# Kernel optimization log

Hardware: AMD Instinct MI355X
Metric: run time of the kernel (lower is better)

## Reference

```python
import jax, jax.numpy as jnp
import numpy as np

B, N, E, H = 4, 2048, 1024, 16
D = E // H
SCALE = D ** -0.5
EPS = 1.1920929e-07  # torch.finfo(float32).eps (RMSNorm default eps=None)


def _rmsnorm(x, w):
    # normalize over last dim (head_dim)
    ms = jnp.mean(x * x, axis=-1, keepdims=True)
    return x * jax.lax.rsqrt(ms + EPS) * w


def setup_inputs() -> dict:
    key = jax.random.key(0)
    ks = jax.random.split(key, 10)
    s_in = E ** -0.5
    return {
        "hidden_states": jax.random.normal(ks[0], (B, N, E), jnp.float32),
        "encoder_hidden_states": jax.random.normal(ks[1], (B, N, E), jnp.float32),
        "Wq": jax.random.normal(ks[2], (E, E), jnp.float32) * s_in,
        "bq": jnp.zeros((E,), jnp.float32),
        "Wkv": jax.random.normal(ks[3], (E, 2 * E), jnp.float32) * s_in,
        "bkv": jnp.zeros((2 * E,), jnp.float32),
        "qn_w": jnp.ones((D,), jnp.float32),
        "kn_w": jnp.ones((D,), jnp.float32),
        "Wo": jax.random.normal(ks[4], (E, E), jnp.float32) * s_in,
        "bo": jnp.zeros((E,), jnp.float32),
    }


def reference(hidden_states, encoder_hidden_states, Wq, bq, Wkv, bkv, qn_w, kn_w, Wo, bo):
    q_proj = hidden_states @ Wq + bq                     # [B,N,E]
    kv_proj = encoder_hidden_states @ Wkv + bkv          # [B,N,2E]
    qkv = jnp.concatenate([q_proj, kv_proj], axis=-1)    # [B,N,3E]
    # Rearrange 'b n (h d j) -> b h n d j' with j=3 innermost: interleaved split
    qkv = qkv.reshape(B, N, H, D, 3)
    q = jnp.transpose(qkv[..., 0], (0, 2, 1, 3)) * SCALE  # [B,H,N,D]
    k = jnp.transpose(qkv[..., 1], (0, 2, 1, 3))
    v = jnp.transpose(qkv[..., 2], (0, 2, 1, 3))
    q = _rmsnorm(q, qn_w)
    k = _rmsnorm(k, kn_w)
    # q already pre-scaled (before norm, which cancels it up to eps); attention uses no extra scale
    scores = jnp.einsum('bhqd,bhkd->bhqk', q, k)          # [B,H,N,N]
    attn = jax.nn.softmax(scores, axis=-1)
    ctx = jnp.einsum('bhqk,bhkd->bhqd', attn, v)          # [B,H,N,D]
    ctx = jnp.transpose(ctx, (0, 2, 1, 3)).reshape(B, N, E)
    return ctx @ Wo + bo
```

## Files before the change

### kernel.cpp

```cpp
#include <hip/hip_runtime.h>
#include <hip/hip_bf16.h>
#include <cstddef>
#include <cmath>

#define B_ 4
#define N_ 2048
#define E_ 1024
#define H_ 16
#define D_ 64
#define SCALE_ 0.125f
#define EPS_ 1.1920929e-07f

typedef __attribute__((ext_vector_type(8))) short short8;
typedef __attribute__((ext_vector_type(4))) short short4s;
typedef __attribute__((ext_vector_type(4))) float floatx4;

__device__ __forceinline__ unsigned short f2bf(float x) {
    unsigned int u = __float_as_uint(x);
    u += 0x7FFFu + ((u >> 16) & 1u);
    return (unsigned short)(u >> 16);
}
__device__ __forceinline__ float bf2f(unsigned short b) {
    return __uint_as_float(((unsigned int)b) << 16);
}

#define MFMA16(a, b, c) __builtin_amdgcn_mfma_f32_16x16x32_bf16((a), (b), (c), 0, 0, 0)

__global__ __launch_bounds__(256) void aprep_kernel(float* __restrict__ x)
{
    const size_t i = ((size_t)blockIdx.x * 256 + threadIdx.x) * 4;
    float4 v = *(const float4*)(x + i);
    float vx[4] = {v.x, v.y, v.z, v.w};
    short8 p;
#pragma unroll
    for (int c = 0; c < 4; ++c) {
        unsigned short hb = f2bf(vx[c]);
        p[2 * c]     = (short)hb;
        p[2 * c + 1] = (short)f2bf(vx[c] - bf2f(hb));
    }
    *(short8*)(x + i) = p;
}

__global__ __launch_bounds__(256) void wtrans_kernel(
    const float* __restrict__ src, int K, int N,
    short* __restrict__ dstH, short* __restrict__ dstL)
{
    __shared__ __align__(16) short Hs[64][68], Ls[64][68];
    const int k0 = blockIdx.x * 64, n0 = blockIdx.y * 64;
    const int t = threadIdx.x;
    {
        int kk = t >> 4, cc = (t & 15) * 4;
#pragma unroll
        for (int i = 0; i < 4; ++i) {
            int k = kk + i * 16;
            float4 v = *(const float4*)(src + (size_t)(k0 + k) * N + n0 + cc);
            float vx[4] = {v.x, v.y, v.z, v.w};
            short4s h4, l4;
#pragma unroll
            for (int c = 0; c < 4; ++c) {
                unsigned short hb = f2bf(vx[c]);
                h4[c] = (short)hb;
                l4[c] = (short)f2bf(vx[c] - bf2f(hb));
            }
            *(short4s*)&Hs[k][cc] = h4;
            *(short4s*)&Ls[k][cc] = l4;
        }
    }
    __syncthreads();
    {
        int nn = t >> 3, kq = (t & 7) * 8;
#pragma unroll
        for (int i = 0; i < 2; ++i) {
            int n = nn + i * 32;
            short8 h8, l8;
#pragma unroll
            for (int j = 0; j < 8; ++j) { h8[j] = Hs[kq + j][n]; l8[j] = Ls[kq + j][n]; }
            *(short8*)(dstH + (size_t)(n0 + n) * K + k0 + kq) = h8;
            *(short8*)(dstL + (size_t)(n0 + n) * K + k0 + kq) = l8;
        }
    }
}

__global__ __launch_bounds__(256) void proj_kernel(
    const short* __restrict__ hs_pk, const short* __restrict__ ehs_pk,
    const short* __restrict__ WtqH, const short* __restrict__ WtqL,
    const short* __restrict__ WtkvH, const short* __restrict__ WtkvL,
    const float* __restrict__ bq, const float* __restrict__ bkv,
    short* __restrict__ qh, short* __restrict__ ql,
    short* __restrict__ kh, short* __restrict__ kl,
    short* __restrict__ vt)
{
    const int ct = blockIdx.x;
    const int rt = blockIdx.y;
    const int col0 = ct * 128;
    const bool isQ = (col0 < 1024);
    const short* __restrict__ Apk  = (isQ ? hs_pk : ehs_pk) + (size_t)rt * 128 * 1024 * 2;
    const short* __restrict__ WH   = isQ ? WtqH : WtkvH;
    const short* __restrict__ WL   = isQ ? WtqL : WtkvL;
    const float* __restrict__ bias = isQ ? bq : bkv;
    const int wcol0 = isQ ? col0 : (col0 - 1024);

    __shared__ __align__(16) short Ah[128 * 40], Al[128 * 40];
    __shared__ __align__(16) short Bh[128 * 40], Bl[128 * 40];

    const int tid = threadIdx.x;
    const int lane = tid & 63, wid = tid >> 6;
    const int wr = wid >> 1, wc = wid & 1;
    const int l15 = lane & 15, g = lane >> 4;

    floatx4 acc[4][4];
#pragma unroll
    for (int m = 0; m < 4; ++m)
#pragma unroll
        for (int n = 0; n < 4; ++n) acc[m][n] = floatx4{0.f, 0.f, 0.f, 0.f};

    short8 rA[4], rBh[2], rBl[2];

    auto LOAD = [&](int k0) {
#pragma unroll
        for (int i = 0; i < 4; ++i) {
            int f = tid + i * 256;
            int row = f >> 3, kq = f & 7;
            rA[i] = *(const short8*)(Apk + ((size_t)row * 1024 + k0 + kq * 4) * 2);
        }
#pragma unroll
        for (int i = 0; i < 2; ++i) {
            int f = tid + i * 256;
            int colb = f >> 2, kq = (f & 3) * 8;
            rBh[i] = *(const short8*)(WH + (size_t)(wcol0 + colb) * 1024 + k0 + kq);
            rBl[i] = *(const short8*)(WL + (size_t)(wcol0 + colb) * 1024 + k0 + kq);
        }
    };
    auto STORE = [&]() {
#pragma unroll
        for (int i = 0; i < 4; ++i) {
            int f = tid + i * 256;
            int row = f >> 3, kq = f & 7;
            short4s h4, l4;
#pragma unroll
            for (int c = 0; c < 4; ++c) { h4[c] = rA[i][2 * c]; l4[c] = rA[i][2 * c + 1]; }
            *(short4s*)&Ah[row * 40 + kq * 4] = h4;
            *(short4s*)&Al[row * 40 + kq * 4] = l4;
        }
#pragma unroll
        for (int i = 0; i < 2; ++i) {
            int f = tid + i * 256;
            int colb = f >> 2, kq = (f & 3) * 8;
            *(short8*)&Bh[colb * 40 + kq] = rBh[i];
            *(short8*)&Bl[colb * 40 + kq] = rBl[i];
        }
    };
    auto COMPUTE = [&]() {
        short8 ah[4], al[4], bh[4], bl[4];
#pragma unroll
        for (int m = 0; m < 4; ++m) {
            int r = (wr * 64 + m * 16 + l15) * 40 + g * 8;
            ah[m] = *(const short8*)&Ah[r];
            al[m] = *(const short8*)&Al[r];
        }
#pragma unroll
        for (int n = 0; n < 4; ++n) {
            int r = (wc * 64 + n * 16 + l15) * 40 + g * 8;
            bh[n] = *(const short8*)&Bh[r];
            bl[n] = *(const short8*)&Bl[r];
        }
#pragma unroll
        for (int m = 0; m < 4; ++m)
#pragma unroll
            for (int n = 0; n < 4; ++n) {
                acc[m][n] = MFMA16(ah[m], bh[n], acc[m][n]);
                acc[m][n] = MFMA16(ah[m], bl[n], acc[m][n]);
                acc[m][n] = MFMA16(al[m], bh[n], acc[m][n]);
            }
    };

    LOAD(0);
    STORE();
    __syncthreads();
    for (int k0 = 32; k0 < 1024; k0 += 32) {
        LOAD(k0);
        COMPUTE();
        __syncthreads();
        STORE();
        __syncthreads();
    }
    COMPUTE();

#pragma unroll
    for (int n = 0; n < 4; ++n) {
        int c = col0 + wc * 64 + n * 16 + l15;
        float bi = bias[c - (isQ ? 0 : 1024)];
        int h   = c / 192;
        int rem = c - h * 192;
        int dd  = rem / 3;
        int j3  = rem - dd * 3;
#pragma unroll
        for (int m = 0; m < 4; ++m) {
            int grow0 = rt * 128 + wr * 64 + m * 16 + g * 4;
            int b = grow0 >> 11, nn0 = grow0 & 2047;
            if (j3 == 2) {
                short4s v4;
#pragma unroll
                for (int r = 0; r < 4; ++r) v4[r] = (short)f2bf(acc[m][n][r] + bi);
                *(short4s*)(vt + (((size_t)b * 16 + h) * 64 + dd) * 2048 + nn0) = v4;
            } else {
                short* dh = (j3 == 0) ? qh : kh;
                short* dl = (j3 == 0) ? ql : kl;
#pragma unroll
                for (int r = 0; r < 4; ++r) {
                    float val = acc[m][n][r] + bi;
                    size_t idx = (((size_t)b * 16 + h) * 2048 + (nn0 + r)) * 64 + dd;
                    unsigned short hb = f2bf(val);
                    dh[idx] = (short)hb;
                    dl[idx] = (short)f2bf(val - bf2f(hb));
                }
            }
        }
    }
}

__global__ __launch_bounds__(256) void rmsnorm_kernel(
    short* __restrict__ qh, short* __restrict__ ql,
    short* __restrict__ kh, short* __restrict__ kl,
    const float* __restrict__ qn_w, const float* __restrict__ kn_w)
{
    const int tid = threadIdx.x, lane = tid & 63, wid = tid >> 6;
    const size_t row = (size_t)blockIdx.x * 16 + wid * 4 + (lane >> 4);
    const int d4 = (lane & 15) * 4;
    const bool isQ = (blockIdx.y == 0);
    short* xh = (isQ ? qh : kh) + row * 64 + d4;
    short* xl = (isQ ? ql : kl) + row * 64 + d4;
    const float* w = (isQ ? qn_w : kn_w) + d4;

    short4s h4 = *(short4s*)xh, l4 = *(short4s*)xl;
    float x[4];
#pragma unroll
    for (int c = 0; c < 4; ++c) {
        x[c] = bf2f((unsigned short)h4[c]) + bf2f((unsigned short)l4[c]);
        if (isQ) x[c] *= SCALE_;
    }
    float s = x[0]*x[0] + x[1]*x[1] + x[2]*x[2] + x[3]*x[3];
#pragma unroll
    for (int off = 1; off <= 8; off <<= 1) s += __shfl_xor(s, off);
    float r = rsqrtf(s * (1.f / 64.f) + EPS_);
#pragma unroll
    for (int c = 0; c < 4; ++c) {
        float y = x[c] * r * w[c];
        unsigned short hb = f2bf(y);
        h4[c] = (short)hb;
        l4[c] = (short)f2bf(y - bf2f(hb));
    }
    *(short4s*)xh = h4;
    *(short4s*)xl = l4;
}

__global__ __launch_bounds__(256) void attn_kernel(
    const short* __restrict__ qh, const short* __restrict__ ql,
    const short* __restrict__ kh, const short* __restrict__ kl,
    const short* __restrict__ vt,
    short* __restrict__ cxh, short* __restrict__ cxl)
{
    const int bh = blockIdx.x;
    const int qt = blockIdx.y;
    const size_t kbase = (size_t)bh * 2048 * 64;
    const size_t vbase = (size_t)bh * 64 * 2048;

    __shared__ __align__(16) short Kh[64 * 72], Kl[64 * 72];
    __shared__ __align__(16) short Vs[64 * 72];
    __shared__ __align__(16) short Ps[64 * 72];

    const int tid = threadIdx.x;
    const int lane = tid & 63, wid = tid >> 6;
    const int l15 = lane & 15, g = lane >> 4;

    const size_t qrow0 = ((size_t)bh * 2048 + qt * 64 + wid * 16 + l15) * 64;
    short8 qfh[2], qfl[2];
#pragma unroll
    for (int s = 0; s < 2; ++s) {
        qfh[s] = *(const short8*)(qh + qrow0 + s * 32 + g * 8);
        qfl[s] = *(const short8*)(ql + qrow0 + s * 32 + g * 8);
    }

    short8 rKh[2], rKl[2], rV[2];
    auto LOADKV = [&](int kt) {
#pragma unroll
        for (int i = 0; i < 2; ++i) {
            int f = tid + i * 256;
            int row = f >> 3, dq = (f & 7) * 8;
            const size_t gsrc = kbase + (size_t)(kt * 64 + row) * 64 + dq;
            rKh[i] = *(const short8*)(kh + gsrc);
            rKl[i] = *(const short8*)(kl + gsrc);
        }
#pragma unroll
        for (int i = 0; i < 2; ++i) {
            int f = tid + i * 256;
            int dd = f >> 3, nq = (f & 7) * 8;
            rV[i] = *(const short8*)(vt + vbase + (size_t)dd * 2048 + kt * 64 + nq);
        }
    };
    auto STOREKV = [&]() {
#pragma unroll
        for (int i = 0; i < 2; ++i) {
            int f = tid + i * 256;
            int row = f >> 3, dq = (f & 7) * 8;
            *(short8*)&Kh[row * 72 + dq] = rKh[i];
            *(short8*)&Kl[row * 72 + dq] = rKl[i];
        }
#pragma unroll
        for (int i = 0; i < 2; ++i) {
            int f = tid + i * 256;
            int dd = f >> 3, nq = (f & 7) * 8;
            *(short8*)&Vs[dd * 72 + nq] = rV[i];
        }
    };

    floatx4 acc_o[4];
#pragma unroll
    for (int n = 0; n < 4; ++n) acc_o[n] = floatx4{0.f, 0.f, 0.f, 0.f};
    float m_i = -INFINITY, l_i = 0.f;

    LOADKV(0);
    for (int kt = 0; kt < 32; ++kt) {
        __syncthreads();
        STOREKV();
        __syncthreads();
        if (kt + 1 < 32) LOADKV(kt + 1);

        floatx4 s4[4];
#pragma unroll
        for (int n = 0; n < 4; ++n) s4[n] = floatx4{0.f, 0.f, 0.f, 0.f};
#pragma unroll
        for (int s = 0; s < 2; ++s)
#pragma unroll
            for (int n = 0; n < 4; ++n) {
                int r = (n * 16 + l15) * 72 + s * 32 + g * 8;
                short8 kfh = *(const short8*)&Kh[r];
                short8 kfl = *(const short8*)&Kl[r];
                s4[n] = MFMA16(kfh, qfh[s], s4[n]);
                s4[n] = MFMA16(kfh, qfl[s], s4[n]);
                s4[n] = MFMA16(kfl, qfh[s], s4[n]);
            }

        float mt = s4[0][0];
#pragma unroll
        for (int n = 0; n < 4; ++n) {
            mt = fmaxf(mt, fmaxf(fmaxf(s4[n][0], s4[n][1]), fmaxf(s4[n][2], s4[n][3])));
        }
        mt = fmaxf(mt, __shfl_xor(mt, 16));
        mt = fmaxf(mt, __shfl_xor(mt, 32));
        float mnew = fmaxf(m_i, mt);
        float corr = __expf(m_i - mnew);
        m_i = mnew;
        float ps = 0.f;
#pragma unroll
        for (int n = 0; n < 4; ++n) {
            short4s p4;
#pragma unroll
            for (int r = 0; r < 4; ++r) {
                float p = __expf(s4[n][r] - mnew);
                unsigned short pbits = f2bf(p);
                p4[r] = (short)pbits;
                ps += bf2f(pbits);
            }
            *(short4s*)&Ps[(wid * 16 + l15) * 72 + n * 16 + g * 4] = p4;
        }
        ps += __shfl_xor(ps, 16);
        ps += __shfl_xor(ps, 32);
        l_i = l_i * corr + ps;

        float corr4[4];
#pragma unroll
        for (int r = 0; r < 4; ++r) corr4[r] = __shfl(corr, g * 4 + r);
#pragma unroll
        for (int n = 0; n < 4; ++n)
#pragma unroll
            for (int r = 0; r < 4; ++r) acc_o[n][r] *= corr4[r];

#pragma unroll
        for (int s = 0; s < 2; ++s) {
            short8 pa = *(const short8*)&Ps[(wid * 16 + l15) * 72 + s * 32 + g * 8];
#pragma unroll
            for (int n = 0; n < 4; ++n) {
                short8 vf = *(const short8*)&Vs[(n * 16 + l15) * 72 + s * 32 + g * 8];
                acc_o[n] = MFMA16(pa, vf, acc_o[n]);
            }
        }
    }

    float inv = 1.f / l_i;
    float inv4[4];
#pragma unroll
    for (int r = 0; r < 4; ++r) inv4[r] = __shfl(inv, g * 4 + r);
    const int b = bh >> 4, h = bh & 15;
#pragma unroll
    for (int r = 0; r < 4; ++r) {
        int row = qt * 64 + wid * 16 + g * 4 + r;
#pragma unroll
        for (int n = 0; n < 4; ++n) {
            float val = acc_o[n][r] * inv4[r];
            size_t o = ((size_t)b * 2048 + row) * 1024 + h * 64 + n * 16 + l15;
            unsigned short hb = f2bf(val);
            cxh[o] = (short)hb;
            cxl[o] = (short)f2bf(val - bf2f(hb));
        }
    }
}

__global__ __launch_bounds__(256) void out_gemm_kernel(
    const short* __restrict__ cxh, const short* __restrict__ cxl,
    const short* __restrict__ WtoH, const short* __restrict__ WtoL,
    const float* __restrict__ bias, float* __restrict__ out)
{
    const int ct = blockIdx.x;
    const int rt = blockIdx.y;
    const int col0 = ct * 128;

    __shared__ __align__(16) short Ah[128 * 40], Al[128 * 40];
    __shared__ __align__(16) short Bh[128 * 40], Bl[128 * 40];

    const int tid = threadIdx.x;
    const int lane = tid & 63, wid = tid >> 6;
    const int wr = wid >> 1, wc = wid & 1;
    const int l15 = lane & 15, g = lane >> 4;

    floatx4 acc[4][4];
#pragma unroll
    for (int m = 0; m < 4; ++m)
#pragma unroll
        for (int n = 0; n < 4; ++n) acc[m][n] = floatx4{0.f, 0.f, 0.f, 0.f};

    short8 rAh[2], rAl[2], rBh[2], rBl[2];

    auto LOAD = [&](int k0) {
#pragma unroll
        for (int i = 0; i < 2; ++i) {
            int f = tid + i * 256;
            int row = f >> 2, kq = (f & 3) * 8;
            const size_t gsrc = (size_t)(rt * 128 + row) * 1024 + k0 + kq;
            rAh[i] = *(const short8*)(cxh + gsrc);
            rAl[i] = *(const short8*)(cxl + gsrc);
        }
#pragma unroll
        for (int i = 0; i < 2; ++i) {
            int f = tid + i * 256;
            int colb = f >> 2, kq = (f & 3) * 8;
            rBh[i] = *(const short8*)(WtoH + (size_t)(col0 + colb) * 1024 + k0 + kq);
            rBl[i] = *(const short8*)(WtoL + (size_t)(col0 + colb) * 1024 + k0 + kq);
        }
    };
    auto STORE = [&]() {
#pragma unroll
        for (int i = 0; i < 2; ++i) {
            int f = tid + i * 256;
            int row = f >> 2, kq = (f & 3) * 8;
            *(short8*)&Ah[row * 40 + kq] = rAh[i];
            *(short8*)&Al[row * 40 + kq] = rAl[i];
        }
#pragma unroll
        for (int i = 0; i < 2; ++i) {
            int f = tid + i * 256;
            int colb = f >> 2, kq = (f & 3) * 8;
            *(short8*)&Bh[colb * 40 + kq] = rBh[i];
            *(short8*)&Bl[colb * 40 + kq] = rBl[i];
        }
    };
    auto COMPUTE = [&]() {
        short8 ah[4], al[4], bh[4], bl[4];
#pragma unroll
        for (int m = 0; m < 4; ++m) {
            int r = (wr * 64 + m * 16 + l15) * 40 + g * 8;
            ah[m] = *(const short8*)&Ah[r];
            al[m] = *(const short8*)&Al[r];
        }
#pragma unroll
        for (int n = 0; n < 4; ++n) {
            int r = (wc * 64 + n * 16 + l15) * 40 + g * 8;
            bh[n] = *(const short8*)&Bh[r];
            bl[n] = *(const short8*)&Bl[r];
        }
#pragma unroll
        for (int m = 0; m < 4; ++m)
#pragma unroll
            for (int n = 0; n < 4; ++n) {
                acc[m][n] = MFMA16(ah[m], bh[n], acc[m][n]);
                acc[m][n] = MFMA16(ah[m], bl[n], acc[m][n]);
                acc[m][n] = MFMA16(al[m], bh[n], acc[m][n]);
            }
    };

    LOAD(0);
    STORE();
    __syncthreads();
    for (int k0 = 32; k0 < 1024; k0 += 32) {
        LOAD(k0);
        COMPUTE();
        __syncthreads();
        STORE();
        __syncthreads();
    }
    COMPUTE();

#pragma unroll
    for (int n = 0; n < 4; ++n) {
        int c = col0 + wc * 64 + n * 16 + l15;
        float bi = bias[c];
#pragma unroll
        for (int m = 0; m < 4; ++m)
#pragma unroll
            for (int r = 0; r < 4; ++r) {
                size_t grow = (size_t)rt * 128 + wr * 64 + m * 16 + g * 4 + r;
                out[grow * 1024 + c] = acc[m][n][r] + bi;
            }
    }
}

extern "C" void kernel_launch(void* const* d_in, const int* in_sizes, int n_in,
                              void* d_out, int out_size, void* d_ws, size_t ws_size,
                              hipStream_t stream)
{
    float* hs  = (float*)d_in[0];
    float* ehs = (float*)d_in[1];
    const float* Wq  = (const float*)d_in[2];
    const float* bq  = (const float*)d_in[3];
    const float* Wkv = (const float*)d_in[4];
    const float* bkv = (const float*)d_in[5];
    const float* qn  = (const float*)d_in[6];
    const float* kn  = (const float*)d_in[7];
    const float* Wo  = (const float*)d_in[8];
    const float* bo  = (const float*)d_in[9];
    float* out = (float*)d_out;

    const size_t SZ = (size_t)B_ * H_ * N_ * D_;
    short* ws   = (short*)d_ws;
    short* qh   = ws;
    short* ql   = qh + SZ;
    short* kh   = ql + SZ;
    short* kl   = kh + SZ;
    short* vt   = kl + SZ;
    short* cxh  = vt + SZ;
    short* cxl  = cxh + SZ;
    short* WtqH = cxl + SZ;
    short* WtqL = WtqH + 1024 * 1024;
    short* WtkvH = WtqL + 1024 * 1024;
    short* WtkvL = WtkvH + 2048 * 1024;
    short* WtoH  = WtkvL + 2048 * 1024;
    short* WtoL  = WtoH + 1024 * 1024;

    aprep_kernel<<<8192, 256, 0, stream>>>(hs);
    aprep_kernel<<<8192, 256, 0, stream>>>(ehs);
    wtrans_kernel<<<dim3(16, 16), 256, 0, stream>>>(Wq, 1024, 1024, WtqH, WtqL);
    wtrans_kernel<<<dim3(16, 32), 256, 0, stream>>>(Wkv, 1024, 2048, WtkvH, WtkvL);
    wtrans_kernel<<<dim3(16, 16), 256, 0, stream>>>(Wo, 1024, 1024, WtoH, WtoL);

    proj_kernel<<<dim3(24, 64), 256, 0, stream>>>((const short*)hs, (const short*)ehs,
                                                  WtqH, WtqL, WtkvH, WtkvL,
                                                  bq, bkv, qh, ql, kh, kl, vt);
    rmsnorm_kernel<<<dim3(8192, 2), 256, 0, stream>>>(qh, ql, kh, kl, qn, kn);
    attn_kernel<<<dim3(64, 32), 256, 0, stream>>>(qh, ql, kh, kl, vt, cxh, cxl);
    out_gemm_kernel<<<dim3(8, 64), 256, 0, stream>>>(cxh, cxl, WtoH, WtoL, bo, out);
}
```

Baseline: 660.6 us.

## Use exp2 with folded log2e, XOR-swizzled LDS, XCD-aware block remap in attention

Folds log2(e) into the normalized Q so the softmax can use the hardware v_exp_f32 (exp2) directly, and packs probabilities with v_cvt_pk_bf16_f32 instead of manual rounding. K and V shared-memory tiles drop the 72-element padding in favor of an XOR swizzle, shrinking LDS while avoiding bank conflicts. The grid is flattened and remapped so consecutive query tiles of one head land on the same XCD, improving L2 reuse of K/V. The hardware cvt rounding and exp2 precision may differ slightly from the previous software path.

```diff
diff --git a/kernel.cpp b/kernel.cpp
--- a/kernel.cpp
+++ b/kernel.cpp
@@ -10,9 +10,11 @@
 #define D_ 64
 #define SCALE_ 0.125f
 #define EPS_ 1.1920929e-07f
+#define LOG2E_ 1.4426950408889634f
 
 typedef __attribute__((ext_vector_type(8))) short short8;
 typedef __attribute__((ext_vector_type(4))) short short4s;
+typedef __attribute__((ext_vector_type(2))) int int2v;
 typedef __attribute__((ext_vector_type(4))) float floatx4;
 
 __device__ __forceinline__ unsigned short f2bf(float x) {
@@ -22,6 +24,16 @@
 }
 __device__ __forceinline__ float bf2f(unsigned short b) {
     return __uint_as_float(((unsigned int)b) << 16);
+}
+__device__ __forceinline__ float exp2_hw(float x) {
+    float r;
+    asm("v_exp_f32 %0, %1" : "=v"(r) : "v"(x));
+    return r;
+}
+__device__ __forceinline__ unsigned int cvtpk_bf16(float lo, float hi) {
+    unsigned int r;
+    asm("v_cvt_pk_bf16_f32 %0, %1, %2" : "=v"(r) : "v"(lo), "v"(hi));
+    return r;
 }
 
 #define MFMA16(a, b, c) __builtin_amdgcn_mfma_f32_16x16x32_bf16((a), (b), (c), 0, 0, 0)
@@ -246,6 +258,7 @@
 #pragma unroll
     for (int c = 0; c < 4; ++c) {
         float y = x[c] * r * w[c];
+        if (isQ) y *= LOG2E_;
         unsigned short hb = f2bf(y);
         h4[c] = (short)hb;
         l4[c] = (short)f2bf(y - bf2f(hb));
@@ -260,13 +273,15 @@
     const short* __restrict__ vt,
     short* __restrict__ cxh, short* __restrict__ cxl)
 {
-    const int bh = blockIdx.x;
-    const int qt = blockIdx.y;
+    const int bid  = blockIdx.x;
+    const int orig = (bid & 7) * 256 + (bid >> 3);
+    const int bh = orig >> 5;
+    const int qt = orig & 31;
     const size_t kbase = (size_t)bh * 2048 * 64;
     const size_t vbase = (size_t)bh * 64 * 2048;
 
-    __shared__ __align__(16) short Kh[64 * 72], Kl[64 * 72];
-    __shared__ __align__(16) short Vs[64 * 72];
+    __shared__ __align__(16) short Kh[64 * 64], Kl[64 * 64];
+    __shared__ __align__(16) short Vs[64 * 64];
     __shared__ __align__(16) short Ps[64 * 72];
 
     const int tid = threadIdx.x;
@@ -302,15 +317,17 @@
 #pragma unroll
         for (int i = 0; i < 2; ++i) {
             int f = tid + i * 256;
-            int row = f >> 3, dq = (f & 7) * 8;
-            *(short8*)&Kh[row * 72 + dq] = rKh[i];
-            *(short8*)&Kl[row * 72 + dq] = rKl[i];
-        }
-#pragma unroll
-        for (int i = 0; i < 2; ++i) {
-            int f = tid + i * 256;
-            int dd = f >> 3, nq = (f & 7) * 8;
-            *(short8*)&Vs[dd * 72 + nq] = rV[i];
+            int row = f >> 3;
+            int sc = ((f & 7) * 16) ^ ((row & 7) << 4);
+            *(short8*)&Kh[row * 64 + (sc >> 1)] = rKh[i];
+            *(short8*)&Kl[row * 64 + (sc >> 1)] = rKl[i];
+        }
+#pragma unroll
+        for (int i = 0; i < 2; ++i) {
+            int f = tid + i * 256;
+            int dd = f >> 3;
+            int sc = ((f & 7) * 16) ^ ((dd & 7) << 4);
+            *(short8*)&Vs[dd * 64 + (sc >> 1)] = rV[i];
         }
     };
 
@@ -333,7 +350,9 @@
         for (int s = 0; s < 2; ++s)
 #pragma unroll
             for (int n = 0; n < 4; ++n) {
-                int r = (n * 16 + l15) * 72 + s * 32 + g * 8;
+                int row = n * 16 + l15;
+                int cb = (s * 64 + g * 16) ^ ((l15 & 7) << 4);
+                int r = row * 64 + (cb >> 1);
                 short8 kfh = *(const short8*)&Kh[r];
                 short8 kfl = *(const short8*)&Kl[r];
                 s4[n] = MFMA16(kfh, qfh[s], s4[n]);
@@ -349,20 +368,17 @@
         mt = fmaxf(mt, __shfl_xor(mt, 16));
         mt = fmaxf(mt, __shfl_xor(mt, 32));
         float mnew = fmaxf(m_i, mt);
-        float corr = __expf(m_i - mnew);
+        float corr = exp2_hw(m_i - mnew);
         m_i = mnew;
         float ps = 0.f;
 #pragma unroll
         for (int n = 0; n < 4; ++n) {
-            short4s p4;
-#pragma unroll
-            for (int r = 0; r < 4; ++r) {
-                float p = __expf(s4[n][r] - mnew);
-                unsigned short pbits = f2bf(p);
-                p4[r] = (short)pbits;
-                ps += bf2f(pbits);
-            }
-            *(short4s*)&Ps[(wid * 16 + l15) * 72 + n * 16 + g * 4] = p4;
+            unsigned int pkA = cvtpk_bf16(exp2_hw(s4[n][0] - mnew), exp2_hw(s4[n][1] - mnew));
+            unsigned int pkB = cvtpk_bf16(exp2_hw(s4[n][2] - mnew), exp2_hw(s4[n][3] - mnew));
+            ps += __uint_as_float(pkA << 16) + __uint_as_float(pkA & 0xffff0000u)
+                + __uint_as_float(pkB << 16) + __uint_as_float(pkB & 0xffff0000u);
+            int2v pk2; pk2[0] = (int)pkA; pk2[1] = (int)pkB;
+            *(int2v*)&Ps[(wid * 16 + l15) * 72 + n * 16 + g * 4] = pk2;
         }
         ps += __shfl_xor(ps, 16);
         ps += __shfl_xor(ps, 32);
@@ -381,7 +397,9 @@
             short8 pa = *(const short8*)&Ps[(wid * 16 + l15) * 72 + s * 32 + g * 8];
 #pragma unroll
             for (int n = 0; n < 4; ++n) {
-                short8 vf = *(const short8*)&Vs[(n * 16 + l15) * 72 + s * 32 + g * 8];
+                int row = n * 16 + l15;
+                int cb = (s * 64 + g * 16) ^ ((l15 & 7) << 4);
+                short8 vf = *(const short8*)&Vs[row * 64 + (cb >> 1)];
                 acc_o[n] = MFMA16(pa, vf, acc_o[n]);
             }
         }
@@ -556,6 +574,6 @@
                                                   WtqH, WtqL, WtkvH, WtkvL,
                                                   bq, bkv, qh, ql, kh, kl, vt);
     rmsnorm_kernel<<<dim3(8192, 2), 256, 0, stream>>>(qh, ql, kh, kl, qn, kn);
-    attn_kernel<<<dim3(64, 32), 256, 0, stream>>>(qh, ql, kh, kl, vt, cxh, cxl);
+    attn_kernel<<<2048, 256, 0, stream>>>(qh, ql, kh, kl, vt, cxh, cxl);
     out_gemm_kernel<<<dim3(8, 64), 256, 0, stream>>>(cxh, cxl, WtoH, WtoL, bo, out);
 }
```

After: 630.4 us. -4.6%, faster.
